# Performance work log

Measured on AMD Instinct MI355X. Metric: run time of the kernel, lower is better.

## Reference

```python
import jax, jax.numpy as jnp
import numpy as np

N, E, DIN, DOUT, H = 50000, 800000, 256, 128, 8
DH = DOUT // H  # per-head dim = 16


def setup_inputs() -> dict:
    key = jax.random.key(0)
    k1, k2, k3, k4, k5 = jax.random.split(key, 5)
    x = jax.random.normal(k1, (N, DIN), dtype=jnp.float32)
    edge_index = jax.random.randint(k2, (2, E), 0, N)
    W_trans = jax.random.normal(k3, (DOUT, DIN), dtype=jnp.float32) / np.sqrt(DIN).astype(np.float32)
    W_att = jax.random.normal(k4, (1, 2 * DH), dtype=jnp.float32) / np.sqrt(2 * DH).astype(np.float32)
    b_att = jax.random.normal(k5, (1,), dtype=jnp.float32) * 0.01
    return {"x": x, "W_trans": W_trans, "W_att": W_att, "b_att": b_att, "edge_index": edge_index}


def reference(x, W_trans, W_att, b_att, edge_index):
    n = x.shape[0]
    # append self-loops (as in the torch module)
    loops = jnp.arange(n, dtype=edge_index.dtype)
    ei = jnp.concatenate([edge_index, jnp.stack([loops, loops])], axis=1)  # [2, E+N]
    src, dst = ei[0], ei[1]

    # linear transform, split heads: [n, H, DH]
    h = (x @ W_trans.T).reshape(n, H, DH)
    h_i = h[src]  # [Etot, H, DH]
    h_j = h[dst]  # [Etot, H, DH]

    # per-edge attention score: concat -> linear -> leaky_relu(0.2)
    s = jnp.concatenate([h_i, h_j], axis=-1) @ W_att.T + b_att  # [Etot, H, 1]
    s = jnp.where(s >= 0, s, 0.2 * s)

    # softmax(dim=0)*exp_sum/scatter_add(exp) == exp(s)/segment_sum(exp(s)) per dst node
    e = jnp.exp(s)
    denom = jax.ops.segment_sum(e, dst, num_segments=n)  # [n, H, 1]
    att = e / denom[dst]

    out = jax.ops.segment_sum(h_i * att, dst, num_segments=n)  # [n, H, DH]
    return out.reshape(n, DOUT)  # head_fusion='cat'
```

## Files before the change

kernel.cpp:

```cpp
#include <hip/hip_runtime.h>


constexpr int DIN  = 256;
constexpr int DOUT = 128;
constexpr int H    = 8;
constexpr int CAP  = 5120;
constexpr int CHUNK = 4096;

typedef __attribute__((ext_vector_type(8))) short bf16x8;
typedef __attribute__((ext_vector_type(4))) float f32x4;

__device__ __forceinline__ float lrelu(float s) { return s >= 0.0f ? s : 0.2f * s; }

__device__ __forceinline__ unsigned short f2bf(float f) {
  unsigned u = __float_as_uint(f);
  u += 0x7FFF + ((u >> 16) & 1);
  return (unsigned short)(u >> 16);
}
__device__ __forceinline__ float bflo(unsigned u) { return __uint_as_float(u << 16); }
__device__ __forceinline__ float bfhi(unsigned u) { return __uint_as_float(u & 0xFFFF0000u); }

__device__ __forceinline__ int wave_incl_scan(int v, int lane) {
#pragma unroll
  for (int d = 1; d < 64; d <<= 1) {
    int t = __shfl_up(v, d, 64);
    if (lane >= d) v += t;
  }
  return v;
}

__global__ void conv_w(const float* __restrict__ W, unsigned short* __restrict__ Wbf,
                       int n, int* __restrict__ bcount, int nb) {
  int i = blockIdx.x * blockDim.x + threadIdx.x;
  if (i < n) Wbf[i] = f2bf(W[i]);
  if (blockIdx.x == 0 && threadIdx.x < nb) bcount[threadIdx.x] = 0;
}

__global__ __launch_bounds__(256) void bp_gemm(const float* __restrict__ x,
                                               const unsigned short* __restrict__ Wbf,
                                               unsigned short* __restrict__ hbf, int N,
                                               const int* __restrict__ ei,
                                               int* __restrict__ bcount,
                                               unsigned* __restrict__ pair_buf,
                                               int E, int nb, int bp_blocks) {
  __shared__ int hist[256];
  __shared__ int gbase[256];
  if ((int)blockIdx.x < bp_blocks) {
    int c0 = blockIdx.x * CHUNK;
    hist[threadIdx.x] = 0;
    __syncthreads();
    int dcache[16];
#pragma unroll
    for (int q = 0; q < 16; ++q) {
      int e = c0 + q * 256 + threadIdx.x;
      dcache[q] = (e < E) ? ei[E + e] : -1;
      if (dcache[q] >= 0) atomicAdd(&hist[dcache[q] >> 8], 1);
    }
    __syncthreads();
    if (threadIdx.x < nb) {
      int c = hist[threadIdx.x];
      gbase[threadIdx.x] = c ? atomicAdd(&bcount[threadIdx.x], c) : 0;
    }
    __syncthreads();
    hist[threadIdx.x] = 0;
    __syncthreads();
#pragma unroll
    for (int q = 0; q < 16; ++q) {
      int e = c0 + q * 256 + threadIdx.x;
      if (dcache[q] >= 0) {
        int s = ei[e];
        int bk = dcache[q] >> 8;
        int r = atomicAdd(&hist[bk], 1);
        pair_buf[bk * CAP + gbase[bk] + r] = ((unsigned)s << 8) | (unsigned)(dcache[q] & 255);
      }
    }
    return;
  }
  int wid = (blockIdx.x - bp_blocks) * 4 + (threadIdx.x >> 6);
  int m0 = wid * 16;
  if (m0 >= N) return;
  int lane = threadIdx.x & 63;
  int mr = lane & 15;
  int kg = lane >> 4;
  int rr = m0 + mr;
  if (rr >= N) rr = N - 1;
  const float* xrow = x + (size_t)rr * DIN + kg * 8;

  f32x4 acc[8];
#pragma unroll
  for (int t = 0; t < 8; ++t) acc[t] = (f32x4){0.f, 0.f, 0.f, 0.f};

#pragma unroll
  for (int ks = 0; ks < 8; ++ks) {
    float4 alo = *(const float4*)(xrow + ks * 32);
    float4 ahi = *(const float4*)(xrow + ks * 32 + 4);
    bf16x8 a;
    a[0] = (short)f2bf(alo.x); a[1] = (short)f2bf(alo.y);
    a[2] = (short)f2bf(alo.z); a[3] = (short)f2bf(alo.w);
    a[4] = (short)f2bf(ahi.x); a[5] = (short)f2bf(ahi.y);
    a[6] = (short)f2bf(ahi.z); a[7] = (short)f2bf(ahi.w);
#pragma unroll
    for (int t = 0; t < 8; ++t) {
      bf16x8 b = *(const bf16x8*)(Wbf + ((size_t)(t * 16 + mr) * DIN + ks * 32 + kg * 8));
      acc[t] = __builtin_amdgcn_mfma_f32_16x16x32_bf16(a, b, acc[t], 0, 0, 0);
    }
  }
#pragma unroll
  for (int t = 0; t < 8; ++t) {
#pragma unroll
    for (int r = 0; r < 4; ++r) {
      int row = m0 + kg * 4 + r;
      if (row < N) hbf[(size_t)row * DOUT + t * 16 + mr] = f2bf(acc[t][r]);
    }
  }
}

__global__ __launch_bounds__(256) void fs_ns(const unsigned* __restrict__ pair_buf,
                                             const int* __restrict__ bcount,
                                             int* __restrict__ offsets,
                                             unsigned short* __restrict__ src_sorted,
                                             const unsigned short* __restrict__ hbf,
                                             const float* __restrict__ Wa,
                                             float* __restrict__ a_src,
                                             float* __restrict__ a_dst,
                                             int N, int E, int nb) {
  __shared__ int cnt[256];
  __shared__ int cur[256];
  __shared__ int redS[256];
  __shared__ int wsumS[4];
  const int t = threadIdx.x;
  if ((int)blockIdx.x >= nb) {
    int idx = ((int)blockIdx.x - nb) * 256 + t;
    if (idx >= N * H) return;
    int v = idx >> 3, hh = idx & 7;
    const unsigned short* hp = hbf + (size_t)v * DOUT + hh * 16;
    uint4 p0 = *(const uint4*)hp;
    uint4 p1 = *(const uint4*)(hp + 8);
    float hv[16];
    hv[0] = bflo(p0.x); hv[1] = bfhi(p0.x); hv[2] = bflo(p0.y); hv[3] = bfhi(p0.y);
    hv[4] = bflo(p0.z); hv[5] = bfhi(p0.z); hv[6] = bflo(p0.w); hv[7] = bfhi(p0.w);
    hv[8] = bflo(p1.x); hv[9] = bfhi(p1.x); hv[10] = bflo(p1.y); hv[11] = bfhi(p1.y);
    hv[12] = bflo(p1.z); hv[13] = bfhi(p1.z); hv[14] = bflo(p1.w); hv[15] = bfhi(p1.w);
    float s1 = 0.f, s2 = 0.f;
#pragma unroll
    for (int d = 0; d < 16; ++d) {
      s1 += hv[d] * Wa[d];
      s2 += hv[d] * Wa[16 + d];
    }
    a_src[idx] = s1;
    a_dst[idx] = s2;
    return;
  }
  const int B = blockIdx.x;
  const int node0 = B * 256;
  const int v = node0 + t;
  const int valid = (v < N);
  cnt[t] = valid ? 1 : 0;
  __syncthreads();
  const int cntE = bcount[B];
  const unsigned* reg = pair_buf + B * CAP;
  for (int i = t; i < cntE; i += 256)
    atomicAdd(&cnt[reg[i] & 255], 1);
  redS[t] = (t < B) ? bcount[t] : 0;
  __syncthreads();
  for (int s = 128; s > 0; s >>= 1) {
    if (t < s) redS[t] += redS[t + s];
    __syncthreads();
  }
  const int csr_base = redS[0] + node0;
  int val = cnt[t];
  int lane = t & 63, wv = t >> 6;
  int inc = wave_incl_scan(val, lane);
  if (lane == 63) wsumS[wv] = inc;
  __syncthreads();
  int base = 0;
  for (int q = 0; q < wv; ++q) base += wsumS[q];
  int ex = base + inc - val;
  cur[t] = ex + 1;
  if (valid) {
    offsets[v] = csr_base + ex;
    src_sorted[csr_base + ex] = (unsigned short)v;
  }
  if (B == 0 && t == 0) offsets[N] = E + N;
  __syncthreads();
  for (int i = t; i < cntE; i += 256) {
    unsigned p = reg[i];
    int k = atomicAdd(&cur[p & 255], 1);
    src_sorted[csr_base + k] = (unsigned short)(p >> 8);
  }
}

__global__ __launch_bounds__(256) void aggregate(const unsigned short* __restrict__ hbf,
                                                 const float* __restrict__ a_src,
                                                 const float* __restrict__ a_dst,
                                                 const float* __restrict__ b_att,
                                                 const int* __restrict__ offsets,
                                                 const unsigned short* __restrict__ src_sorted,
                                                 float* __restrict__ out, int N) {
  int wid = blockIdx.x * 4 + (threadIdx.x >> 6);
  if (wid >= N) return;
  int lane = threadIdx.x & 63;
  int g = lane >> 4, sl = lane & 15;
  int head = sl >> 1;
  float adv = a_dst[wid * H + head] + b_att[0];
  int beg = offsets[wid], end = offsets[wid + 1];
  float a0 = 0, a1 = 0, a2 = 0, a3 = 0, a4 = 0, a5 = 0, a6 = 0, a7 = 0, den = 0;
  for (int j0 = beg; j0 < end; j0 += 8) {
    int ja = j0 + g, jb = j0 + 4 + g;
    bool va = ja < end, vb = jb < end;
    int sa = src_sorted[va ? ja : beg];
    int sb = src_sorted[vb ? jb : beg];
    float asa = a_src[sa * H + head];
    float asb = a_src[sb * H + head];
    uint4 ua = *(const uint4*)(hbf + sa * DOUT + sl * 8);
    uint4 ub = *(const uint4*)(hbf + sb * DOUT + sl * 8);
    float ea = va ? __expf(lrelu(asa + adv)) : 0.f;
    float eb = vb ? __expf(lrelu(asb + adv)) : 0.f;
    den += ea + eb;
    a0 += ea * bflo(ua.x) + eb * bflo(ub.x);
    a1 += ea * bfhi(ua.x) + eb * bfhi(ub.x);
    a2 += ea * bflo(ua.y) + eb * bflo(ub.y);
    a3 += ea * bfhi(ua.y) + eb * bfhi(ub.y);
    a4 += ea * bflo(ua.z) + eb * bflo(ub.z);
    a5 += ea * bfhi(ua.z) + eb * bfhi(ub.z);
    a6 += ea * bflo(ua.w) + eb * bflo(ub.w);
    a7 += ea * bfhi(ua.w) + eb * bfhi(ub.w);
  }
  den += __shfl_xor(den, 16, 64); den += __shfl_xor(den, 32, 64);
  a0 += __shfl_xor(a0, 16, 64); a0 += __shfl_xor(a0, 32, 64);
  a1 += __shfl_xor(a1, 16, 64); a1 += __shfl_xor(a1, 32, 64);
  a2 += __shfl_xor(a2, 16, 64); a2 += __shfl_xor(a2, 32, 64);
  a3 += __shfl_xor(a3, 16, 64); a3 += __shfl_xor(a3, 32, 64);
  a4 += __shfl_xor(a4, 16, 64); a4 += __shfl_xor(a4, 32, 64);
  a5 += __shfl_xor(a5, 16, 64); a5 += __shfl_xor(a5, 32, 64);
  a6 += __shfl_xor(a6, 16, 64); a6 += __shfl_xor(a6, 32, 64);
  a7 += __shfl_xor(a7, 16, 64); a7 += __shfl_xor(a7, 32, 64);
  float inv = 1.0f / den;
  if (g == 0) {
    float4 o = make_float4(a0 * inv, a1 * inv, a2 * inv, a3 * inv);
    *(float4*)&out[wid * DOUT + sl * 8] = o;
  } else if (g == 1) {
    float4 o = make_float4(a4 * inv, a5 * inv, a6 * inv, a7 * inv);
    *(float4*)&out[wid * DOUT + sl * 8 + 4] = o;
  }
}

extern "C" void kernel_launch(void* const* d_in, const int* in_sizes, int n_in,
                              void* d_out, int out_size, void* d_ws, size_t ws_size,
                              hipStream_t stream) {
  const float* x     = (const float*)d_in[0];
  const float* W     = (const float*)d_in[1];
  const float* Wa    = (const float*)d_in[2];
  const float* b_att = (const float*)d_in[3];
  const int*   ei    = (const int*)d_in[4];
  const int N  = in_sizes[0] / DIN;
  const int E  = in_sizes[4] / 2;
  const int NB = (N + 255) / 256;
  float* out = (float*)d_out;

  char* p = (char*)d_ws;
  auto take = [&p](size_t bytes) {
    uintptr_t u = ((uintptr_t)p + 15) & ~(uintptr_t)15;
    p = (char*)(u + bytes);
    return (void*)u;
  };
  unsigned short* hbf = (unsigned short*)take((size_t)N * DOUT * 2);
  unsigned short* Wbf = (unsigned short*)take((size_t)DOUT * DIN * 2);
  float* a_src        = (float*)take((size_t)N * H * 4);
  float* a_dst        = (float*)take((size_t)N * H * 4);
  int* bcount         = (int*)take((size_t)NB * 4);
  unsigned* pair_buf  = (unsigned*)take((size_t)NB * CAP * 4);
  int* offsets        = (int*)take((size_t)(N + 1) * 4);
  unsigned short* src_sorted = (unsigned short*)take((size_t)(E + N + 16) * 2);

  dim3 b256(256);
  const int bp_blocks   = (E + CHUNK - 1) / CHUNK;
  const int gemm_blocks = ((N + 15) / 16 + 3) / 4;
  const int ns_blocks   = (N * H + 255) / 256;

  conv_w<<<dim3((DOUT * DIN + 255) / 256), b256, 0, stream>>>(W, Wbf, DOUT * DIN, bcount, NB);
  bp_gemm<<<dim3(bp_blocks + gemm_blocks), b256, 0, stream>>>(
      x, Wbf, hbf, N, ei, bcount, pair_buf, E, NB, bp_blocks);
  fs_ns<<<dim3(NB + ns_blocks), b256, 0, stream>>>(
      pair_buf, bcount, offsets, src_sorted, hbf, Wa, a_src, a_dst, N, E, NB);
  aggregate<<<dim3((N + 3) / 4), b256, 0, stream>>>(hbf, a_src, a_dst, b_att, offsets,
                                                    src_sorted, out, N);
}
```

Baseline: 189.3 us.

## Stage bf16 weights in LDS and compute two row tiles per wave

The GEMM part of the fused bucket/GEMM kernel now copies the whole bf16 weight matrix into shared memory once per block, pre-swizzled into MFMA fragment order. Each wave then handles 32 rows instead of 16, reusing every B fragment for two MFMAs, and the next x chunk is prefetched one k-step ahead. This cuts redundant global weight reads and halves the number of GEMM blocks. In exchange, each block uses 64KB of LDS, which limits occupancy to about two blocks per CU, and that limit also applies to the edge-bucketing blocks that share the kernel. Each block also pays a weight-copy prologue.

```diff
diff --git a/kernel.cpp b/kernel.cpp
--- a/kernel.cpp
+++ b/kernel.cpp
@@ -36,16 +36,17 @@
   if (blockIdx.x == 0 && threadIdx.x < nb) bcount[threadIdx.x] = 0;
 }
 
-__global__ __launch_bounds__(256) void bp_gemm(const float* __restrict__ x,
-                                               const unsigned short* __restrict__ Wbf,
-                                               unsigned short* __restrict__ hbf, int N,
-                                               const int* __restrict__ ei,
-                                               int* __restrict__ bcount,
-                                               unsigned* __restrict__ pair_buf,
-                                               int E, int nb, int bp_blocks) {
-  __shared__ int hist[256];
-  __shared__ int gbase[256];
+__global__ __launch_bounds__(256, 2) void bp_gemm(const float* __restrict__ x,
+                                                  const unsigned short* __restrict__ Wbf,
+                                                  unsigned short* __restrict__ hbf, int N,
+                                                  const int* __restrict__ ei,
+                                                  int* __restrict__ bcount,
+                                                  unsigned* __restrict__ pair_buf,
+                                                  int E, int nb, int bp_blocks) {
+  __shared__ __align__(16) unsigned short Wlds[DOUT * DIN];
   if ((int)blockIdx.x < bp_blocks) {
+    int* hist  = (int*)Wlds;
+    int* gbase = hist + 256;
     int c0 = blockIdx.x * CHUNK;
     hist[threadIdx.x] = 0;
     __syncthreads();
@@ -76,43 +77,69 @@
     }
     return;
   }
-  int wid = (blockIdx.x - bp_blocks) * 4 + (threadIdx.x >> 6);
-  int m0 = wid * 16;
+  {
+    const int tid = threadIdx.x;
+#pragma unroll
+    for (int i = 0; i < 16; ++i) {
+      int c = i * 256 + tid;
+      int t = c >> 9, ks = (c >> 6) & 7, L = c & 63;
+      const unsigned short* gp = Wbf + ((t * 16 + (L & 15)) * DIN + ks * 32 + (L >> 4) * 8);
+      *(bf16x8*)&Wlds[c * 8] = *(const bf16x8*)gp;
+    }
+  }
+  __syncthreads();
+  int wid = ((int)blockIdx.x - bp_blocks) * 4 + (threadIdx.x >> 6);
+  int m0 = wid * 32;
   if (m0 >= N) return;
   int lane = threadIdx.x & 63;
-  int mr = lane & 15;
-  int kg = lane >> 4;
-  int rr = m0 + mr;
-  if (rr >= N) rr = N - 1;
-  const float* xrow = x + (size_t)rr * DIN + kg * 8;
-
-  f32x4 acc[8];
-#pragma unroll
-  for (int t = 0; t < 8; ++t) acc[t] = (f32x4){0.f, 0.f, 0.f, 0.f};
-
+  int mr = lane & 15, kg = lane >> 4;
+  int r0 = m0 + mr;       if (r0 >= N) r0 = N - 1;
+  int r1 = m0 + 16 + mr;  if (r1 >= N) r1 = N - 1;
+  const float* xr0 = x + (size_t)r0 * DIN + kg * 8;
+  const float* xr1 = x + (size_t)r1 * DIN + kg * 8;
+  const unsigned short* fb = Wlds + lane * 8;
+
+  f32x4 acc[2][8];
+#pragma unroll
+  for (int mt = 0; mt < 2; ++mt)
+#pragma unroll
+    for (int t = 0; t < 8; ++t) acc[mt][t] = (f32x4){0.f, 0.f, 0.f, 0.f};
+
+  float4 p00 = *(const float4*)xr0, p01 = *(const float4*)(xr0 + 4);
+  float4 p10 = *(const float4*)xr1, p11 = *(const float4*)(xr1 + 4);
 #pragma unroll
   for (int ks = 0; ks < 8; ++ks) {
-    float4 alo = *(const float4*)(xrow + ks * 32);
-    float4 ahi = *(const float4*)(xrow + ks * 32 + 4);
-    bf16x8 a;
-    a[0] = (short)f2bf(alo.x); a[1] = (short)f2bf(alo.y);
-    a[2] = (short)f2bf(alo.z); a[3] = (short)f2bf(alo.w);
-    a[4] = (short)f2bf(ahi.x); a[5] = (short)f2bf(ahi.y);
-    a[6] = (short)f2bf(ahi.z); a[7] = (short)f2bf(ahi.w);
+    bf16x8 a0, a1;
+    a0[0] = (short)f2bf(p00.x); a0[1] = (short)f2bf(p00.y);
+    a0[2] = (short)f2bf(p00.z); a0[3] = (short)f2bf(p00.w);
+    a0[4] = (short)f2bf(p01.x); a0[5] = (short)f2bf(p01.y);
+    a0[6] = (short)f2bf(p01.z); a0[7] = (short)f2bf(p01.w);
+    a1[0] = (short)f2bf(p10.x); a1[1] = (short)f2bf(p10.y);
+    a1[2] = (short)f2bf(p10.z); a1[3] = (short)f2bf(p10.w);
+    a1[4] = (short)f2bf(p11.x); a1[5] = (short)f2bf(p11.y);
+    a1[6] = (short)f2bf(p11.z); a1[7] = (short)f2bf(p11.w);
+    if (ks < 7) {
+      p00 = *(const float4*)(xr0 + (ks + 1) * 32);
+      p01 = *(const float4*)(xr0 + (ks + 1) * 32 + 4);
+      p10 = *(const float4*)(xr1 + (ks + 1) * 32);
+      p11 = *(const float4*)(xr1 + (ks + 1) * 32 + 4);
+    }
 #pragma unroll
     for (int t = 0; t < 8; ++t) {
-      bf16x8 b = *(const bf16x8*)(Wbf + ((size_t)(t * 16 + mr) * DIN + ks * 32 + kg * 8));
-      acc[t] = __builtin_amdgcn_mfma_f32_16x16x32_bf16(a, b, acc[t], 0, 0, 0);
-    }
-  }
-#pragma unroll
-  for (int t = 0; t < 8; ++t) {
-#pragma unroll
-    for (int r = 0; r < 4; ++r) {
-      int row = m0 + kg * 4 + r;
-      if (row < N) hbf[(size_t)row * DOUT + t * 16 + mr] = f2bf(acc[t][r]);
-    }
-  }
+      bf16x8 b = *(const bf16x8*)(fb + ((t * 8 + ks) << 9));
+      acc[0][t] = __builtin_amdgcn_mfma_f32_16x16x32_bf16(a0, b, acc[0][t], 0, 0, 0);
+      acc[1][t] = __builtin_amdgcn_mfma_f32_16x16x32_bf16(a1, b, acc[1][t], 0, 0, 0);
+    }
+  }
+#pragma unroll
+  for (int mt = 0; mt < 2; ++mt)
+#pragma unroll
+    for (int t = 0; t < 8; ++t)
+#pragma unroll
+      for (int r = 0; r < 4; ++r) {
+        int row = m0 + mt * 16 + kg * 4 + r;
+        if (row < N) hbf[(size_t)row * DOUT + t * 16 + mr] = f2bf(acc[mt][t][r]);
+      }
 }
 
 __global__ __launch_bounds__(256) void fs_ns(const unsigned* __restrict__ pair_buf,
@@ -275,7 +302,7 @@
 
   dim3 b256(256);
   const int bp_blocks   = (E + CHUNK - 1) / CHUNK;
-  const int gemm_blocks = ((N + 15) / 16 + 3) / 4;
+  const int gemm_blocks = ((N + 31) / 32 + 3) / 4;
   const int ns_blocks   = (N * H + 255) / 256;
 
   conv_w<<<dim3((DOUT * DIN + 255) / 256), b256, 0, stream>>>(W, Wbf, DOUT * DIN, bcount, NB);
```

Result: faster. 172.0 us (-9.1%).
